# Optimization experiments

Hardware: AMD Instinct MI355X
Metric: run time of the kernel (lower is better)

Reference implementation:

```python
import jax, jax.numpy as jnp
import numpy as np

D_MODEL = 1024
N_HEADS = 16
HEAD_DIM = D_MODEL // N_HEADS
EPS = 1e-6


def setup_inputs() -> dict:
    key = jax.random.key(0)
    ks = jax.random.split(key, 10)
    s = 0.02
    return {
        "sequence": jax.random.normal(ks[0], (4, 2048, D_MODEL), dtype=jnp.float32),
        "ln_gamma": jnp.ones((D_MODEL,), jnp.float32),
        "ln_beta": jnp.zeros((D_MODEL,), jnp.float32),
        "Wq": jax.random.normal(ks[1], (D_MODEL, D_MODEL), jnp.float32) * s,
        "bq": jnp.zeros((D_MODEL,), jnp.float32),
        "Wk": jax.random.normal(ks[2], (D_MODEL, D_MODEL), jnp.float32) * s,
        "bk": jnp.zeros((D_MODEL,), jnp.float32),
        "Wv": jax.random.normal(ks[3], (D_MODEL, D_MODEL), jnp.float32) * s,
        "bv": jnp.zeros((D_MODEL,), jnp.float32),
        "Wo": jax.random.normal(ks[4], (D_MODEL, D_MODEL), jnp.float32) * s,
        "bo": jnp.zeros((D_MODEL,), jnp.float32),
        "mu": jnp.zeros((1, 1, 1, 1), jnp.float32),
    }


def _split_heads(x):
    b, s, d = x.shape
    return x.reshape(b, s, N_HEADS, HEAD_DIM).transpose(0, 2, 1, 3)  # [B,H,S,hd]


def reference(sequence, ln_gamma, ln_beta, Wq, bq, Wk, bk, Wv, bv, Wo, bo, mu):
    # LayerNorm (eps=1e-6)
    mean = jnp.mean(sequence, axis=-1, keepdims=True)
    var = jnp.mean(jnp.square(sequence - mean), axis=-1, keepdims=True)
    x = (sequence - mean) / jnp.sqrt(var + EPS) * ln_gamma + ln_beta

    # QKV projections (torch Linear: x @ W.T + b)
    q = _split_heads(x @ Wq.T + bq)
    k = _split_heads(x @ Wk.T + bk)
    v = _split_heads(x @ Wv.T + bv)

    scale = HEAD_DIM ** 0.5
    scores = jnp.einsum("bhqd,bhkd->bhqk", q, k) / scale  # [B,H,S,S]
    scores = jax.nn.sigmoid(scores - mu) * jnp.exp(scores)
    scores = scores / jnp.sum(scores, axis=-1, keepdims=True)

    out = jnp.einsum("bhqk,bhkd->bhqd", scores, v)  # [B,H,S,hd]
    b, h, s, hd = out.shape
    out = out.transpose(0, 2, 1, 3).reshape(b, s, h * hd)
    return out @ Wo.T + bo  # dropout is identity at inference
```

## Files before the change

kernel.cpp:

```cpp
#include <hip/hip_runtime.h>
#include <hip/hip_bf16.h>
#include <cstdint>
#include <cstddef>


typedef __bf16 bf16_t;
typedef __bf16 bf16x4 __attribute__((ext_vector_type(4)));
typedef __bf16 bf16x8 __attribute__((ext_vector_type(8)));
typedef float  f32x2  __attribute__((ext_vector_type(2)));
typedef float  f32x4  __attribute__((ext_vector_type(4)));
typedef float  f32x16 __attribute__((ext_vector_type(16)));
typedef unsigned u32x4 __attribute__((ext_vector_type(4)));

#define MFMA16(a, b, c) __builtin_amdgcn_mfma_f32_16x16x32_bf16((a), (b), (c), 0, 0, 0)
#define MFMA32(a, b, c) __builtin_amdgcn_mfma_f32_32x32x16_bf16((a), (b), (c), 0, 0, 0)

#if __has_builtin(__builtin_amdgcn_exp2f)
#define VEXP2(x) __builtin_amdgcn_exp2f(x)
#else
#define VEXP2(x) __expf((x) * 0.6931471805599453f)
#endif

__device__ __forceinline__ unsigned cvtpk_bf16(float a, float b) {
  unsigned r;
  asm("v_cvt_pk_bf16_f32 %0, %1, %2" : "=v"(r) : "v"(a), "v"(b));
  return r;
}

__device__ __forceinline__ void plane32_swap(unsigned& a, unsigned& b) {
  asm volatile("v_permlane32_swap_b32 %0, %1" : "+v"(a), "+v"(b));
}

__device__ __forceinline__ void gload16(void* lds, const void* g) {
  __builtin_amdgcn_global_load_lds(
      (__attribute__((address_space(1))) void*)(uintptr_t)g,
      (__attribute__((address_space(3))) void*)(uint32_t)(uintptr_t)lds,
      16, 0, 0);
}

__global__ __launch_bounds__(256) void cvt_w_k(
    const float* __restrict__ s0, const float* __restrict__ s1,
    const float* __restrict__ s2, const float* __restrict__ s3,
    bf16_t* __restrict__ dst)
{
  const float* src = blockIdx.y == 0 ? s0 : blockIdx.y == 1 ? s1
                   : blockIdx.y == 2 ? s2 : s3;
  int i = blockIdx.x * 256 + threadIdx.x;
  float4 v = ((const float4*)src)[i];
  bf16x4 o = { (bf16_t)v.x, (bf16_t)v.y, (bf16_t)v.z, (bf16_t)v.w };
  *(bf16x4*)(dst + (((size_t)blockIdx.y) << 20) + (size_t)i * 4) = o;
}

__global__ __launch_bounds__(256) void ln_k(
    const float* __restrict__ x, const float* __restrict__ gamma,
    const float* __restrict__ beta, bf16_t* __restrict__ out)
{
  int row = blockIdx.x;
  int tid = threadIdx.x;
  float4 v = ((const float4*)(x + (size_t)row * 1024))[tid];
  float s  = v.x + v.y + v.z + v.w;
  float ss = v.x * v.x + v.y * v.y + v.z * v.z + v.w * v.w;
#pragma unroll
  for (int m = 1; m < 64; m <<= 1) { s += __shfl_xor(s, m); ss += __shfl_xor(ss, m); }
  __shared__ float sh_s[4], sh_q[4];
  int w = tid >> 6;
  if ((tid & 63) == 0) { sh_s[w] = s; sh_q[w] = ss; }
  __syncthreads();
  s  = sh_s[0] + sh_s[1] + sh_s[2] + sh_s[3];
  ss = sh_q[0] + sh_q[1] + sh_q[2] + sh_q[3];
  float mean = s * (1.0f / 1024.0f);
  float var  = ss * (1.0f / 1024.0f) - mean * mean;
  float rstd = rsqrtf(var + 1e-6f);
  float4 gv = ((const float4*)gamma)[tid];
  float4 bv = ((const float4*)beta)[tid];
  bf16x4 o = { (bf16_t)((v.x - mean) * rstd * gv.x + bv.x),
               (bf16_t)((v.y - mean) * rstd * gv.y + bv.y),
               (bf16_t)((v.z - mean) * rstd * gv.z + bv.z),
               (bf16_t)((v.w - mean) * rstd * gv.w + bv.w) };
  *(bf16x4*)(out + (size_t)row * 1024 + tid * 4) = o;
}

__global__ __launch_bounds__(256) void gemm_bt(
    const bf16_t* __restrict__ A, const bf16_t* __restrict__ Bw,
    const float* __restrict__ b0, const float* __restrict__ b1,
    const float* __restrict__ b2,
    void* __restrict__ o0, void* __restrict__ o1, void* __restrict__ o2,
    int M, int N, int K, int fused)
{
  __shared__ __align__(16) bf16_t a_lds[2][128][32];
  __shared__ __align__(16) bf16_t b_lds[2][128][32];
  const int tid = threadIdx.x;
  const int l = tid & 63, w = tid >> 6;
  const int wr = w >> 1, wc = w & 1;
  const int m0 = blockIdx.y * 128, n0 = blockIdx.x * 128;
  const int lr = l & 15, lg = l >> 4;

  f32x4 acc[4][4] = {};

  const int srow = tid >> 2;
  const int scol = (tid & 3) * 8;
  const bf16_t* ag = A  + (size_t)(m0 + srow) * K + scol;
  const bf16_t* bg = Bw + (size_t)(n0 + srow) * K + scol;

  gload16((char*)a_lds[0] + tid * 16,        ag);
  gload16((char*)a_lds[0] + 4096 + tid * 16, ag + (size_t)64 * K);
  gload16((char*)b_lds[0] + tid * 16,        bg);
  gload16((char*)b_lds[0] + 4096 + tid * 16, bg + (size_t)64 * K);
  __syncthreads();

  int cur = 0;
  for (int k0 = 0; k0 < K; k0 += 32) {
    if (k0 + 32 < K) {
      gload16((char*)a_lds[cur ^ 1] + tid * 16,        ag + k0 + 32);
      gload16((char*)a_lds[cur ^ 1] + 4096 + tid * 16, ag + (size_t)64 * K + k0 + 32);
      gload16((char*)b_lds[cur ^ 1] + tid * 16,        bg + k0 + 32);
      gload16((char*)b_lds[cur ^ 1] + 4096 + tid * 16, bg + (size_t)64 * K + k0 + 32);
    }
    bf16x8 af[4], bf[4];
#pragma unroll
    for (int i = 0; i < 4; ++i) {
      af[i] = *(const bf16x8*)&a_lds[cur][wr * 64 + i * 16 + lr][lg * 8];
      bf[i] = *(const bf16x8*)&b_lds[cur][wc * 64 + i * 16 + lr][lg * 8];
    }
#pragma unroll
    for (int i = 0; i < 4; ++i)
#pragma unroll
      for (int j = 0; j < 4; ++j)
        acc[i][j] = MFMA16(af[i], bf[j], acc[i][j]);
    __syncthreads();
    cur ^= 1;
  }

  int matsel = fused ? (n0 >> 10) : 0;
  const float* bias = matsel == 0 ? b0 : matsel == 1 ? b1 : b2;
  float bs[4];
#pragma unroll
  for (int j = 0; j < 4; ++j) bs[j] = bias[(n0 + wc * 64 + j * 16 + lr) & 1023];

#pragma unroll
  for (int i = 0; i < 4; ++i) {
#pragma unroll
    for (int j = 0; j < 4; ++j) {
      if (fused && matsel == 2) {
        int row0 = m0 + wr * 64 + i * 16 + lg * 4;
        int col  = n0 + wc * 64 + j * 16 + lr;
        int nn = col & 1023;
        int bb = row0 >> 11, s0 = row0 & 2047, hh = nn >> 6, d = nn & 63;
        bf16x4 pv;
#pragma unroll
        for (int r = 0; r < 4; ++r) pv[r] = (bf16_t)(acc[i][j][r] + bs[j]);
        *(bf16x4*)((bf16_t*)o2 + ((((size_t)bb * 16 + hh) * 64) + d) * 2048 + s0) = pv;
      } else {
#pragma unroll
        for (int r = 0; r < 4; ++r) {
          int row = m0 + wr * 64 + i * 16 + lg * 4 + r;
          int col = n0 + wc * 64 + j * 16 + lr;
          float v = acc[i][j][r] + bs[j];
          if (!fused) {
            ((float*)o0)[(size_t)row * N + col] = v;
          } else {
            int nn = col & 1023;
            int bb = row >> 11, s = row & 2047, hh = nn >> 6, d = nn & 63;
            bf16_t* o = matsel ? (bf16_t*)o1 : (bf16_t*)o0;
            if (matsel == 0) v *= 0.18033688011112042f;
            o[((((size_t)bb * 16 + hh) * 2048 + s) << 6) + d] = (bf16_t)v;
          }
        }
      }
    }
  }
}

__global__ __launch_bounds__(256) void attn_k(
    const bf16_t* __restrict__ q, const bf16_t* __restrict__ k,
    const bf16_t* __restrict__ vT, const float* __restrict__ mu_p,
    bf16_t* __restrict__ out)
{
  const int S = 2048;
  int hw = blockIdx.x;
  int vid = (hw & 7) * 128 + (hw >> 3);
  int qt = vid & 15;
  int bh = vid >> 4;
  int h = bh & 15, b = bh >> 4;

  const bf16_t* qb = q  + ((size_t)bh * S + qt * 128) * 64;
  const char* kbase = (const char*)(k  + (size_t)bh * S * 64);
  const char* vbase = (const char*)(vT + (size_t)bh * 64 * S);
  const float emu = __expf(mu_p[0]);
  const f32x2 emu2 = { emu, emu };

  __shared__ __align__(16) bf16_t k_lds[2][64][64];
  __shared__ __align__(16) bf16_t v_lds[2][64][64];

  const int tid = threadIdx.x, l = tid & 63, w = tid >> 6;
  const int l31 = l & 31, hi = l >> 5;
  const int swzr = (l31 & 7) << 4;

  bf16x8 qf[4];
#pragma unroll
  for (int ch = 0; ch < 4; ++ch)
    qf[ch] = *(const bf16x8*)(qb + (size_t)(w * 32 + l31) * 64 + ch * 16 + hi * 8);

  const int srow = tid >> 3;
  const int ssw  = ((tid & 7) * 16) ^ ((srow & 7) << 4);
  const int koff = srow * 128 + ssw;
  const int voff = srow * 4096 + ssw;

  f32x16 oAcc[2] = {};
  f32x2 rsum2 = { 0.f, 0.f };

#pragma unroll
  for (int c = 0; c < 2; ++c) {
    gload16((char*)k_lds[0] + c * 4096 + tid * 16, kbase + koff + c * 4096);
    gload16((char*)v_lds[0] + c * 4096 + tid * 16, vbase + voff + c * 131072);
  }
  __syncthreads();

#pragma unroll 2
  for (int t = 0; t < 32; ++t) {
    const int cur = t & 1;
    if (t + 1 < 32) {
#pragma unroll
      for (int c = 0; c < 2; ++c) {
        gload16((char*)k_lds[cur ^ 1] + c * 4096 + tid * 16,
                kbase + koff + c * 4096 + (t + 1) * 8192);
        gload16((char*)v_lds[cur ^ 1] + c * 4096 + tid * 16,
                vbase + voff + c * 131072 + (t + 1) * 128);
      }
    }

#pragma unroll
    for (int kh = 0; kh < 2; ++kh) {
      f32x16 sc = {};
      __builtin_amdgcn_s_setprio(1);
#pragma unroll
      for (int ch = 0; ch < 4; ++ch) {
        bf16x8 kf = *(const bf16x8*)((const char*)k_lds[cur]
                      + (kh * 32 + l31) * 128 + ((ch * 32 + hi * 16) ^ swzr));
        sc = MFMA32(kf, qf[ch], sc);
      }
      __builtin_amdgcn_s_setprio(0);

      unsigned U[8];
#pragma unroll
      for (int m = 0; m < 8; ++m) {
        f32x2 tt = { VEXP2(-sc[2 * m]), VEXP2(-sc[2 * m + 1]) };
        f32x2 dd = (emu2 * tt) * tt + tt;
        f32x2 ww = { __builtin_amdgcn_rcpf(dd[0]), __builtin_amdgcn_rcpf(dd[1]) };
        rsum2 += ww;
        U[m] = cvtpk_bf16(ww[0], ww[1]);
      }
      plane32_swap(U[0], U[2]);
      plane32_swap(U[1], U[3]);
      plane32_swap(U[4], U[6]);
      plane32_swap(U[5], U[7]);
      __builtin_amdgcn_s_setprio(1);
#pragma unroll
      for (int cc = 0; cc < 2; ++cc) {
        u32x4 uu = { U[cc * 4 + 0], U[cc * 4 + 1], U[cc * 4 + 2], U[cc * 4 + 3] };
        bf16x8 pa = __builtin_bit_cast(bf16x8, uu);
        int kcol = (kh * 2 + cc) * 32 + hi * 16;
#pragma unroll
        for (int df = 0; df < 2; ++df) {
          bf16x8 vf = *(const bf16x8*)((const char*)v_lds[cur]
                        + (df * 32 + l31) * 128 + (kcol ^ swzr));
          oAcc[df] = MFMA32(pa, vf, oAcc[df]);
        }
      }
      __builtin_amdgcn_s_setprio(0);
    }
    __syncthreads();
  }

  float rs = rsum2[0] + rsum2[1];
  rs += __shfl_xor(rs, 32);
  float rinv = __builtin_amdgcn_rcpf(rs);

#pragma unroll
  for (int r = 0; r < 16; ++r) {
    int q_loc = (r & 3) + 8 * (r >> 2) + 4 * hi;
    float ro = __shfl(rinv, q_loc);
    size_t row = (size_t)b * 2048 + qt * 128 + w * 32 + q_loc;
#pragma unroll
    for (int df = 0; df < 2; ++df) {
      out[row * 1024 + h * 64 + df * 32 + l31] = (bf16_t)(oAcc[df][r] * ro);
    }
  }
}

extern "C" void kernel_launch(void* const* d_in, const int* in_sizes, int n_in,
                              void* d_out, int out_size, void* d_ws, size_t ws_size,
                              hipStream_t stream) {
  const float* seq = (const float*)d_in[0];
  const float* g   = (const float*)d_in[1];
  const float* be  = (const float*)d_in[2];
  const float* Wq  = (const float*)d_in[3];
  const float* bq  = (const float*)d_in[4];
  const float* Wk  = (const float*)d_in[5];
  const float* bk  = (const float*)d_in[6];
  const float* Wv  = (const float*)d_in[7];
  const float* bv  = (const float*)d_in[8];
  const float* Wo  = (const float*)d_in[9];
  const float* bo  = (const float*)d_in[10];
  const float* mu  = (const float*)d_in[11];

  char* ws = (char*)d_ws;
  bf16_t* xb   = (bf16_t*)ws;  ws += (size_t)8192 * 1024 * 2;
  bf16_t* wAll = (bf16_t*)ws;  ws += (size_t)4 * 1024 * 1024 * 2;
  bf16_t* qb   = (bf16_t*)ws;  ws += (size_t)8192 * 1024 * 2;
  bf16_t* kbuf = (bf16_t*)ws;  ws += (size_t)8192 * 1024 * 2;
  bf16_t* vtb  = (bf16_t*)ws;  ws += (size_t)8192 * 1024 * 2;
  bf16_t* ab   = (bf16_t*)ws;  ws += (size_t)8192 * 1024 * 2;
  bf16_t* wqkv = wAll;
  bf16_t* wob  = wAll + (size_t)3 * 1024 * 1024;

  dim3 blk(256);
  cvt_w_k<<<dim3(1024, 4), blk, 0, stream>>>(Wq, Wk, Wv, Wo, wAll);
  ln_k<<<dim3(8192), blk, 0, stream>>>(seq, g, be, xb);
  gemm_bt<<<dim3(24, 64), blk, 0, stream>>>(xb, wqkv, bq, bk, bv,
                                            qb, kbuf, vtb, 8192, 3072, 1024, 1);
  attn_k<<<dim3(1024), blk, 0, stream>>>(qb, kbuf, vtb, mu, ab);
  gemm_bt<<<dim3(8, 64), blk, 0, stream>>>(ab, wob, bo, nullptr, nullptr,
                                           d_out, nullptr, nullptr, 8192, 1024, 1024, 0);
}
```

Baseline: 218.4 us.

## Double query rows per attention block to reuse K/V tiles across two sub-tiles

Each attention block now handles 256 query rows (64 per wave, as two 32-row sub-tiles) instead of 128, and the grid shrinks from 1024 to 512 blocks. Every K fragment and V fragment loaded from LDS feeds two MFMAs, which halves global and LDS K/V traffic per query row. The cost is roughly double the accumulator and score registers per wave, which may lower occupancy. With 512 blocks on 256 CUs there is less parallel slack, so the tail and load balance may suffer.

```diff
diff --git a/kernel.cpp b/kernel.cpp
--- a/kernel.cpp
+++ b/kernel.cpp
@@ -178,12 +178,12 @@
 {
   const int S = 2048;
   int hw = blockIdx.x;
-  int vid = (hw & 7) * 128 + (hw >> 3);
-  int qt = vid & 15;
-  int bh = vid >> 4;
+  int vid = (hw & 7) * 64 + (hw >> 3);
+  int qt = vid & 7;
+  int bh = vid >> 3;
   int h = bh & 15, b = bh >> 4;
 
-  const bf16_t* qb = q  + ((size_t)bh * S + qt * 128) * 64;
+  const bf16_t* qb = q  + ((size_t)bh * S + qt * 256) * 64;
   const char* kbase = (const char*)(k  + (size_t)bh * S * 64);
   const char* vbase = (const char*)(vT + (size_t)bh * 64 * S);
   const float emu = __expf(mu_p[0]);
@@ -196,18 +196,21 @@
   const int l31 = l & 31, hi = l >> 5;
   const int swzr = (l31 & 7) << 4;
 
-  bf16x8 qf[4];
-#pragma unroll
-  for (int ch = 0; ch < 4; ++ch)
-    qf[ch] = *(const bf16x8*)(qb + (size_t)(w * 32 + l31) * 64 + ch * 16 + hi * 8);
+  bf16x8 qf[2][4];
+#pragma unroll
+  for (int sub = 0; sub < 2; ++sub)
+#pragma unroll
+    for (int ch = 0; ch < 4; ++ch)
+      qf[sub][ch] = *(const bf16x8*)(qb + (size_t)(w * 64 + sub * 32 + l31) * 64
+                                     + ch * 16 + hi * 8);
 
   const int srow = tid >> 3;
   const int ssw  = ((tid & 7) * 16) ^ ((srow & 7) << 4);
   const int koff = srow * 128 + ssw;
   const int voff = srow * 4096 + ssw;
 
-  f32x16 oAcc[2] = {};
-  f32x2 rsum2 = { 0.f, 0.f };
+  f32x16 oAcc[2][2] = {};
+  f32x2 rsum2[2] = {};
 
 #pragma unroll
   for (int c = 0; c < 2; ++c) {
@@ -231,40 +234,53 @@
 
 #pragma unroll
     for (int kh = 0; kh < 2; ++kh) {
-      f32x16 sc = {};
+      bf16x8 kf[4];
+#pragma unroll
+      for (int ch = 0; ch < 4; ++ch)
+        kf[ch] = *(const bf16x8*)((const char*)k_lds[cur]
+                   + (kh * 32 + l31) * 128 + ((ch * 32 + hi * 16) ^ swzr));
+
+      f32x16 sc[2] = {};
       __builtin_amdgcn_s_setprio(1);
 #pragma unroll
       for (int ch = 0; ch < 4; ++ch) {
-        bf16x8 kf = *(const bf16x8*)((const char*)k_lds[cur]
-                      + (kh * 32 + l31) * 128 + ((ch * 32 + hi * 16) ^ swzr));
-        sc = MFMA32(kf, qf[ch], sc);
+        sc[0] = MFMA32(kf[ch], qf[0][ch], sc[0]);
+        sc[1] = MFMA32(kf[ch], qf[1][ch], sc[1]);
       }
       __builtin_amdgcn_s_setprio(0);
 
-      unsigned U[8];
-#pragma unroll
-      for (int m = 0; m < 8; ++m) {
-        f32x2 tt = { VEXP2(-sc[2 * m]), VEXP2(-sc[2 * m + 1]) };
-        f32x2 dd = (emu2 * tt) * tt + tt;
-        f32x2 ww = { __builtin_amdgcn_rcpf(dd[0]), __builtin_amdgcn_rcpf(dd[1]) };
-        rsum2 += ww;
-        U[m] = cvtpk_bf16(ww[0], ww[1]);
-      }
-      plane32_swap(U[0], U[2]);
-      plane32_swap(U[1], U[3]);
-      plane32_swap(U[4], U[6]);
-      plane32_swap(U[5], U[7]);
+      unsigned U[2][8];
+#pragma unroll
+      for (int sub = 0; sub < 2; ++sub) {
+#pragma unroll
+        for (int m = 0; m < 8; ++m) {
+          f32x2 tt = { VEXP2(-sc[sub][2 * m]), VEXP2(-sc[sub][2 * m + 1]) };
+          f32x2 dd = (emu2 * tt) * tt + tt;
+          f32x2 ww = { __builtin_amdgcn_rcpf(dd[0]), __builtin_amdgcn_rcpf(dd[1]) };
+          rsum2[sub] += ww;
+          U[sub][m] = cvtpk_bf16(ww[0], ww[1]);
+        }
+        plane32_swap(U[sub][0], U[sub][2]);
+        plane32_swap(U[sub][1], U[sub][3]);
+        plane32_swap(U[sub][4], U[sub][6]);
+        plane32_swap(U[sub][5], U[sub][7]);
+      }
+
       __builtin_amdgcn_s_setprio(1);
 #pragma unroll
       for (int cc = 0; cc < 2; ++cc) {
-        u32x4 uu = { U[cc * 4 + 0], U[cc * 4 + 1], U[cc * 4 + 2], U[cc * 4 + 3] };
-        bf16x8 pa = __builtin_bit_cast(bf16x8, uu);
         int kcol = (kh * 2 + cc) * 32 + hi * 16;
 #pragma unroll
         for (int df = 0; df < 2; ++df) {
           bf16x8 vf = *(const bf16x8*)((const char*)v_lds[cur]
                         + (df * 32 + l31) * 128 + (kcol ^ swzr));
-          oAcc[df] = MFMA32(pa, vf, oAcc[df]);
+#pragma unroll
+          for (int sub = 0; sub < 2; ++sub) {
+            u32x4 uu = { U[sub][cc * 4 + 0], U[sub][cc * 4 + 1],
+                         U[sub][cc * 4 + 2], U[sub][cc * 4 + 3] };
+            bf16x8 pa = __builtin_bit_cast(bf16x8, uu);
+            oAcc[sub][df] = MFMA32(pa, vf, oAcc[sub][df]);
+          }
         }
       }
       __builtin_amdgcn_s_setprio(0);
@@ -272,18 +288,20 @@
     __syncthreads();
   }
 
-  float rs = rsum2[0] + rsum2[1];
-  rs += __shfl_xor(rs, 32);
-  float rinv = __builtin_amdgcn_rcpf(rs);
-
-#pragma unroll
-  for (int r = 0; r < 16; ++r) {
-    int q_loc = (r & 3) + 8 * (r >> 2) + 4 * hi;
-    float ro = __shfl(rinv, q_loc);
-    size_t row = (size_t)b * 2048 + qt * 128 + w * 32 + q_loc;
-#pragma unroll
-    for (int df = 0; df < 2; ++df) {
-      out[row * 1024 + h * 64 + df * 32 + l31] = (bf16_t)(oAcc[df][r] * ro);
+#pragma unroll
+  for (int sub = 0; sub < 2; ++sub) {
+    float rs = rsum2[sub][0] + rsum2[sub][1];
+    rs += __shfl_xor(rs, 32);
+    float rinv = __builtin_amdgcn_rcpf(rs);
+#pragma unroll
+    for (int r = 0; r < 16; ++r) {
+      int q_loc = (r & 3) + 8 * (r >> 2) + 4 * hi;
+      float ro = __shfl(rinv, q_loc);
+      size_t row = (size_t)b * 2048 + qt * 256 + w * 64 + sub * 32 + q_loc;
+#pragma unroll
+      for (int df = 0; df < 2; ++df) {
+        out[row * 1024 + h * 64 + df * 32 + l31] = (bf16_t)(oAcc[sub][df][r] * ro);
+      }
     }
   }
 }
@@ -319,7 +337,7 @@
   ln_k<<<dim3(8192), blk, 0, stream>>>(seq, g, be, xb);
   gemm_bt<<<dim3(24, 64), blk, 0, stream>>>(xb, wqkv, bq, bk, bv,
                                             qb, kbuf, vtb, 8192, 3072, 1024, 1);
-  attn_k<<<dim3(1024), blk, 0, stream>>>(qb, kbuf, vtb, mu, ab);
+  attn_k<<<dim3(512), blk, 0, stream>>>(qb, kbuf, vtb, mu, ab);
   gemm_bt<<<dim3(8, 64), blk, 0, stream>>>(ab, wob, bo, nullptr, nullptr,
                                            d_out, nullptr, nullptr, 8192, 1024, 1024, 0);
 }
```

Result: no change. 214.9 us (-1.6%).
